# Optimization experiments

Hardware: AMD Instinct MI355X
Metric: run time of the kernel (lower is better)

Reference implementation:

```python
import jax, jax.numpy as jnp
import numpy as np

B, D, C = 128, 2048, 16522
BETA, KNN, ALPHA0 = 0.05, 6, 0.01


def setup_inputs() -> dict:
    key = jax.random.key(0)
    k1, k2, k3 = jax.random.split(key, 3)
    inputs = jax.random.normal(k1, (B, D), dtype=jnp.float32)
    label = jax.random.randint(k2, (B,), 0, C, dtype=jnp.int64 if jax.config.jax_enable_x64 else jnp.int32)
    # memory bank; init as unit-norm rows (torch init is zeros, but rows are
    # always renormalized after the first update, so unit-norm is the steady state)
    em = jax.random.normal(k3, (C, D), dtype=jnp.float32)
    em = em / jnp.linalg.norm(em, axis=1, keepdims=True)
    return {"inputs": inputs, "label": label, "em": em, "epoch": 10}


def reference(inputs, label, em, epoch):
    alpha = ALPHA0 * epoch
    # similarity logits: [B, C]
    logits = jnp.matmul(inputs, em.T) / BETA
    # smooth_hot mask: 2 at top-k entries, 3 at the true label (overwrites)
    _, topk = jax.lax.top_k(logits, KNN)                      # [B, KNN]
    rows = jnp.arange(B)
    mask = jnp.zeros_like(logits).at[rows[:, None], topk].set(2.0)
    mask = mask.at[rows, label].set(3.0)
    logp = jax.nn.log_softmax(logits, axis=1)
    loss = (-(mask * logp)).sum(axis=1).mean()
    # sequential per-sample EMA memory update (duplicate labels chain, so scan)
    def step(em_cur, xy):
        x, y = xy
        row = alpha * em_cur[y] + (1.0 - alpha) * x
        row = row / jnp.linalg.norm(row)
        return em_cur.at[y].set(row), None
    em_new, _ = jax.lax.scan(step, em, (inputs, label))
    return loss, em_new
```

## Files before the change

kernel.cpp:

```cpp
#include <hip/hip_runtime.h>
#include <hip/hip_bf16.h>
#include <cstddef>

#define B_    128
#define D_    2048
#define C_    16522
#define BETA_INV 20.0f
#define LSTRIDE 16528

#define NTILES 1033
#define NCHUNK 8
#define CHW    2066

typedef __bf16 bf16;
typedef bf16  bf16x8 __attribute__((ext_vector_type(8)));
typedef float f32x4  __attribute__((ext_vector_type(4)));

#define WS_APACK_OFF 8462336
#define WS_PART_OFF  8986624

__global__ __launch_bounds__(256) void pack_a(const float* __restrict__ inp,
                                              bf16* __restrict__ ap) {
  const int tid  = blockIdx.x * 256 + threadIdx.x;
  const int lane = tid & 63;
  const int ks   = (tid >> 6) & 63;
  const int mt   = tid >> 12;
  const int row  = mt * 16 + (lane & 15);
  const int col  = ks * 32 + (lane >> 4) * 8;
  const float4 v0 = *(const float4*)(inp + row * D_ + col);
  const float4 v1 = *(const float4*)(inp + row * D_ + col + 4);
  bf16x8 b;
  b[0] = (bf16)v0.x; b[1] = (bf16)v0.y; b[2] = (bf16)v0.z; b[3] = (bf16)v0.w;
  b[4] = (bf16)v1.x; b[5] = (bf16)v1.y; b[6] = (bf16)v1.z; b[7] = (bf16)v1.w;
  ((bf16x8*)ap)[tid] = b;
}

__global__ __launch_bounds__(256) void copy_em(const float* __restrict__ em,
                                               float* __restrict__ out_em) {
  const size_t n = (size_t)C_ * D_ / 4;
  const size_t stride = (size_t)gridDim.x * 512;
  for (size_t i = (size_t)blockIdx.x * 512 + threadIdx.x; i < n; i += stride) {
    const f32x4 v0 = ((const f32x4*)em)[i];
    const bool  h1 = (i + 256) < n;
    f32x4 v1 = {};
    if (h1) v1 = ((const f32x4*)em)[i + 256];
    ((f32x4*)out_em)[i] = v0;
    if (h1) ((f32x4*)out_em)[i + 256] = v1;
  }
}

__global__ __launch_bounds__(256, 4) void gemm_logits(
    const bf16*  __restrict__ ap,
    const float* __restrict__ em,
    float*       __restrict__ logits)
{
  const int tid  = threadIdx.x;
  const int lane = tid & 63;
  const int w    = tid >> 6;
  const int ml   = lane & 15;
  const int quad = lane >> 4;
  const int n0   = blockIdx.x * 16;
  const int r    = n0 + ml;
  const bool valid = r < C_;

  const float* bp = em + (size_t)(valid ? r : 0) * D_ + quad * 8;
  const bf16x8* af = (const bf16x8*)ap;

  const int ks0 = w * 16;

  f32x4 acc[8] = {};

  f32x4 e0a = *(const f32x4*)(bp + ks0 * 32);
  f32x4 e0b = *(const f32x4*)(bp + ks0 * 32 + 4);

  #pragma unroll 3
  for (int i = 0; i < 15; ++i) {
    const int ks = ks0 + i;
    bf16x8 A0[8];
    #pragma unroll
    for (int mt = 0; mt < 8; ++mt)
      A0[mt] = af[(mt * 64 + ks) * 64 + lane];
    const f32x4 e1a = *(const f32x4*)(bp + (ks + 1) * 32);
    const f32x4 e1b = *(const f32x4*)(bp + (ks + 1) * 32 + 4);
    bf16x8 bv;
    bv[0] = (bf16)e0a[0]; bv[1] = (bf16)e0a[1]; bv[2] = (bf16)e0a[2]; bv[3] = (bf16)e0a[3];
    bv[4] = (bf16)e0b[0]; bv[5] = (bf16)e0b[1]; bv[6] = (bf16)e0b[2]; bv[7] = (bf16)e0b[3];
    #pragma unroll
    for (int mt = 0; mt < 8; ++mt)
      acc[mt] = __builtin_amdgcn_mfma_f32_16x16x32_bf16(A0[mt], bv, acc[mt], 0, 0, 0);
    e0a = e1a; e0b = e1b;
  }
  {
    const int ks = ks0 + 15;
    bf16x8 A0[8];
    #pragma unroll
    for (int mt = 0; mt < 8; ++mt)
      A0[mt] = af[(mt * 64 + ks) * 64 + lane];
    bf16x8 bv;
    bv[0] = (bf16)e0a[0]; bv[1] = (bf16)e0a[1]; bv[2] = (bf16)e0a[2]; bv[3] = (bf16)e0a[3];
    bv[4] = (bf16)e0b[0]; bv[5] = (bf16)e0b[1]; bv[6] = (bf16)e0b[2]; bv[7] = (bf16)e0b[3];
    #pragma unroll
    for (int mt = 0; mt < 8; ++mt)
      acc[mt] = __builtin_amdgcn_mfma_f32_16x16x32_bf16(A0[mt], bv, acc[mt], 0, 0, 0);
  }

  __shared__ f32x4 red[3][8][64];
  if (w > 0) {
    #pragma unroll
    for (int mt = 0; mt < 8; ++mt) red[w - 1][mt][lane] = acc[mt];
  }
  __syncthreads();
  if (w == 0 && valid) {
    #pragma unroll
    for (int mt = 0; mt < 8; ++mt) {
      f32x4 a = acc[mt];
      a += red[0][mt][lane];
      a += red[1][mt][lane];
      a += red[2][mt][lane];
      #pragma unroll
      for (int reg = 0; reg < 4; ++reg) {
        const int row = mt * 16 + quad * 4 + reg;
        logits[row * LSTRIDE + r] = a[reg] * BETA_INV;
      }
    }
  }
}

__global__ __launch_bounds__(256) void row_loss_part(
    const float* __restrict__ logits,
    const int*   __restrict__ label,
    float*       __restrict__ part)
{
  const int b = blockIdx.x >> 3;
  const int c = blockIdx.x & 7;
  const int t = threadIdx.x;
  const int lo = c * CHW;
  const int hi = (lo + CHW < C_) ? lo + CHW : C_;
  const float* row = logits + b * LSTRIDE;
  const int y = label[b];

  float m = -INFINITY, s = 0.f, ly = -INFINITY;
  float tv[6]; int ti[6];
  #pragma unroll
  for (int q = 0; q < 6; ++q) { tv[q] = -INFINITY; ti[q] = -1; }

  for (int i = lo + t; i < hi; i += 256) {
    const float v = row[i];
    if (v > m) { s = s * __expf(m - v) + 1.f; m = v; }
    else       { s += __expf(v - m); }
    if (i == y) ly = v;
    if (v > tv[5]) {
      tv[5] = v; ti[5] = i;
      #pragma unroll
      for (int q = 5; q > 0; --q)
        if (tv[q] > tv[q - 1]) {
          const float fv = tv[q]; tv[q] = tv[q - 1]; tv[q - 1] = fv;
          const int   fi = ti[q]; ti[q] = ti[q - 1]; ti[q - 1] = fi;
        }
    }
  }

  __shared__ float rm[256], rs[256];
  __shared__ float cv[1536];
  __shared__ int   ci[1536];
  __shared__ float sly;

  rm[t] = m; rs[t] = s;
  #pragma unroll
  for (int q = 0; q < 6; ++q) { cv[t * 6 + q] = tv[q]; ci[t * 6 + q] = ti[q]; }
  if (t == 0) sly = -INFINITY;
  __syncthreads();
  if (ly != -INFINITY) sly = ly;

  for (int off = 128; off >= 1; off >>= 1) {
    if (t < off) {
      const float m2 = rm[t + off], s2 = rs[t + off];
      const float M = fmaxf(rm[t], m2);
      rs[t] = rs[t] * __expf(rm[t] - M) + s2 * __expf(m2 - M);
      rm[t] = M;
    }
    __syncthreads();
  }

  if (t < 64) {
    float otv[6]; int oti[6];
    for (int rr = 0; rr < 6; ++rr) {
      float bv = -INFINITY; int bi = -1, bs = -1;
      for (int u = 0; u < 24; ++u) {
        const int slot = t * 24 + u;
        const float v = cv[slot];
        if (v > bv) { bv = v; bi = ci[slot]; bs = slot; }
      }
      #pragma unroll
      for (int off = 32; off >= 1; off >>= 1) {
        const float ov = __shfl_down(bv, off);
        const int   oi = __shfl_down(bi, off);
        const int   os = __shfl_down(bs, off);
        if (ov > bv) { bv = ov; bi = oi; bs = os; }
      }
      bv = __shfl(bv, 0); bi = __shfl(bi, 0); bs = __shfl(bs, 0);
      if (bs >= t * 24 && bs < (t + 1) * 24) cv[bs] = -INFINITY;
      otv[rr] = bv; oti[rr] = bi;
    }
    if (t == 0) {
      float* p = part + (size_t)(b * 8 + c) * 16;
      p[0] = rm[0]; p[1] = rs[0]; p[2] = sly;
      #pragma unroll
      for (int q = 0; q < 6; ++q) { p[4 + q] = otv[q]; ((int*)p)[10 + q] = oti[q]; }
    }
  }
}

__global__ __launch_bounds__(64) void row_loss_merge(
    const float* __restrict__ part,
    const int*   __restrict__ label,
    float*       __restrict__ out)
{
  const int b = blockIdx.x;
  const int lane = threadIdx.x;
  const int y = label[b];

  float m = -INFINITY, s = 0.f, ly = -INFINITY;
  if (lane < 8) {
    const float* p = part + (size_t)(b * 8 + lane) * 16;
    m = p[0]; s = p[1]; ly = p[2];
  }
  float M = m, LY = ly;
  #pragma unroll
  for (int off = 32; off >= 1; off >>= 1) {
    M  = fmaxf(M,  __shfl_down(M,  off));
    LY = fmaxf(LY, __shfl_down(LY, off));
  }
  M = __shfl(M, 0); LY = __shfl(LY, 0);
  float contrib = (lane < 8) ? s * __expf(m - M) : 0.f;
  #pragma unroll
  for (int off = 32; off >= 1; off >>= 1) contrib += __shfl_down(contrib, off);
  const float S = __shfl(contrib, 0);

  float v = -INFINITY; int idx = -1;
  if (lane < 48) {
    const float* p = part + (size_t)(b * 8 + lane / 6) * 16;
    v   = p[4 + lane % 6];
    idx = ((const int*)p)[10 + lane % 6];
  }
  float stop = 0.f; int intop = 0;
  for (int rr = 0; rr < 6; ++rr) {
    float bv = v; int bi = idx, bl = lane;
    #pragma unroll
    for (int off = 32; off >= 1; off >>= 1) {
      const float ov = __shfl_down(bv, off);
      const int   oi = __shfl_down(bi, off);
      const int   ol = __shfl_down(bl, off);
      if (ov > bv) { bv = ov; bi = oi; bl = ol; }
    }
    bv = __shfl(bv, 0); bi = __shfl(bi, 0); bl = __shfl(bl, 0);
    stop += bv;
    if (bi == y) intop = 1;
    if (lane == bl) v = -INFINITY;
  }

  if (lane == 0) {
    const float lse = M + logf(S);
    const float loss = intop ? (13.f * lse - LY - 2.f * stop)
                             : (15.f * lse - 3.f * LY - 2.f * stop);
    atomicAdd(out, loss * (1.0f / 128.0f));
  }
}

__global__ __launch_bounds__(256) void em_update(
    const float* __restrict__ inp,
    const int*   __restrict__ label,
    const float* __restrict__ em,
    const int*   __restrict__ epoch,
    float*       __restrict__ out_em)
{
  __shared__ int lbl[B_];
  __shared__ float red[4];
  const int t = threadIdx.x;
  if (t < B_) lbl[t] = label[t];
  __syncthreads();

  const int i = blockIdx.x;
  const int y = lbl[i];
  for (int j = 0; j < i; ++j)
    if (lbl[j] == y) return;

  const float alpha = 0.01f * (float)epoch[0];
  const int lane = t & 63, wave = t >> 6;

  float r[8];
  #pragma unroll
  for (int u = 0; u < 8; ++u) r[u] = em[(size_t)y * D_ + t + u * 256];

  for (int j = i; j < B_; ++j) {
    if (lbl[j] != y) continue;
    const float* x = inp + j * D_;
    float ss = 0.f;
    #pragma unroll
    for (int u = 0; u < 8; ++u) {
      r[u] = alpha * r[u] + (1.f - alpha) * x[t + u * 256];
      ss += r[u] * r[u];
    }
    #pragma unroll
    for (int off = 32; off >= 1; off >>= 1) ss += __shfl_down(ss, off);
    if (lane == 0) red[wave] = ss;
    __syncthreads();
    const float inv = 1.f / sqrtf(red[0] + red[1] + red[2] + red[3]);
    #pragma unroll
    for (int u = 0; u < 8; ++u) r[u] *= inv;
    __syncthreads();
  }

  #pragma unroll
  for (int u = 0; u < 8; ++u) out_em[(size_t)y * D_ + t + u * 256] = r[u];
}

extern "C" void kernel_launch(void* const* d_in, const int* in_sizes, int n_in,
                              void* d_out, int out_size, void* d_ws, size_t ws_size,
                              hipStream_t stream) {
  const float* inp   = (const float*)d_in[0];
  const int*   label = (const int*)d_in[1];
  const float* em    = (const float*)d_in[2];
  const int*   epoch = (const int*)d_in[3];

  float* out    = (float*)d_out;
  float* out_em = out + 1;
  float* logits = (float*)d_ws;
  bf16*  apack  = (bf16*)((char*)d_ws + WS_APACK_OFF);
  float* part   = (float*)((char*)d_ws + WS_PART_OFF);

  hipMemsetAsync(d_out, 0, sizeof(float), stream);

  pack_a        <<<dim3(128),        dim3(256), 0, stream>>>(inp, apack);
  copy_em       <<<dim3(2048),       dim3(256), 0, stream>>>(em, out_em);
  gemm_logits   <<<dim3(NTILES),     dim3(256), 0, stream>>>(apack, em, logits);
  row_loss_part <<<dim3(B_ * NCHUNK),dim3(256), 0, stream>>>(logits, label, part);
  row_loss_merge<<<dim3(B_),         dim3(64),  0, stream>>>(part, label, out);
  em_update     <<<dim3(B_),         dim3(256), 0, stream>>>(inp, label, em, epoch, out_em);
}
```

Baseline: 130.3 us.

## Fuse em copy into GEMM launch and merge loss-merge with em update

Interleaves the memory-bank copy blocks with the GEMM tile blocks in one launch: of every three blocks, two copy and one computes a tile. The copy and the GEMM both stream em, so running them together can overlap the bandwidth-bound copy with compute and shares em reads in cache. The row-loss merge and the EMA update are also merged into one launch, which removes two kernel launches. The cost is a bigger, mixed kernel whose register budget is set by the GEMM path, and less control over block scheduling.

```diff
diff --git a/kernel.cpp b/kernel.cpp
--- a/kernel.cpp
+++ b/kernel.cpp
@@ -11,6 +11,9 @@
 #define NTILES 1033
 #define NCHUNK 8
 #define CHW    2066
+
+#define NCOPY  2066
+#define NFUSED 3099
 
 typedef __bf16 bf16;
 typedef bf16  bf16x8 __attribute__((ext_vector_type(8)));
@@ -35,31 +38,38 @@
   ((bf16x8*)ap)[tid] = b;
 }
 
-__global__ __launch_bounds__(256) void copy_em(const float* __restrict__ em,
-                                               float* __restrict__ out_em) {
-  const size_t n = (size_t)C_ * D_ / 4;
-  const size_t stride = (size_t)gridDim.x * 512;
-  for (size_t i = (size_t)blockIdx.x * 512 + threadIdx.x; i < n; i += stride) {
-    const f32x4 v0 = ((const f32x4*)em)[i];
-    const bool  h1 = (i + 256) < n;
-    f32x4 v1 = {};
-    if (h1) v1 = ((const f32x4*)em)[i + 256];
-    ((f32x4*)out_em)[i] = v0;
-    if (h1) ((f32x4*)out_em)[i + 256] = v1;
-  }
-}
-
-__global__ __launch_bounds__(256, 4) void gemm_logits(
+__global__ __launch_bounds__(256, 4) void fused_main(
+    const float* __restrict__ em,
+    float*       __restrict__ out_em,
     const bf16*  __restrict__ ap,
-    const float* __restrict__ em,
     float*       __restrict__ logits)
 {
+  const int b  = blockIdx.x;
+  const int g  = b / 3;
+  const int r3 = b - g * 3;
+
+  if (r3 < 2) {
+    const int id = g * 2 + r3;
+    const int t  = threadIdx.x;
+    const size_t n = (size_t)C_ * D_ / 4;
+    const size_t stride = (size_t)NCOPY * 512;
+    for (size_t i = (size_t)id * 512 + t; i < n; i += stride) {
+      const f32x4 v0 = ((const f32x4*)em)[i];
+      const bool  h1 = (i + 256) < n;
+      f32x4 v1 = {};
+      if (h1) v1 = ((const f32x4*)em)[i + 256];
+      ((f32x4*)out_em)[i] = v0;
+      if (h1) ((f32x4*)out_em)[i + 256] = v1;
+    }
+    return;
+  }
+
   const int tid  = threadIdx.x;
   const int lane = tid & 63;
   const int w    = tid >> 6;
   const int ml   = lane & 15;
   const int quad = lane >> 4;
-  const int n0   = blockIdx.x * 16;
+  const int n0   = g * 16;
   const int r    = n0 + ml;
   const bool valid = r < C_;
 
@@ -211,76 +221,77 @@
   }
 }
 
-__global__ __launch_bounds__(64) void row_loss_merge(
+__global__ __launch_bounds__(256) void tail(
     const float* __restrict__ part,
     const int*   __restrict__ label,
-    float*       __restrict__ out)
-{
-  const int b = blockIdx.x;
-  const int lane = threadIdx.x;
-  const int y = label[b];
-
-  float m = -INFINITY, s = 0.f, ly = -INFINITY;
-  if (lane < 8) {
-    const float* p = part + (size_t)(b * 8 + lane) * 16;
-    m = p[0]; s = p[1]; ly = p[2];
-  }
-  float M = m, LY = ly;
-  #pragma unroll
-  for (int off = 32; off >= 1; off >>= 1) {
-    M  = fmaxf(M,  __shfl_down(M,  off));
-    LY = fmaxf(LY, __shfl_down(LY, off));
-  }
-  M = __shfl(M, 0); LY = __shfl(LY, 0);
-  float contrib = (lane < 8) ? s * __expf(m - M) : 0.f;
-  #pragma unroll
-  for (int off = 32; off >= 1; off >>= 1) contrib += __shfl_down(contrib, off);
-  const float S = __shfl(contrib, 0);
-
-  float v = -INFINITY; int idx = -1;
-  if (lane < 48) {
-    const float* p = part + (size_t)(b * 8 + lane / 6) * 16;
-    v   = p[4 + lane % 6];
-    idx = ((const int*)p)[10 + lane % 6];
-  }
-  float stop = 0.f; int intop = 0;
-  for (int rr = 0; rr < 6; ++rr) {
-    float bv = v; int bi = idx, bl = lane;
-    #pragma unroll
-    for (int off = 32; off >= 1; off >>= 1) {
-      const float ov = __shfl_down(bv, off);
-      const int   oi = __shfl_down(bi, off);
-      const int   ol = __shfl_down(bl, off);
-      if (ov > bv) { bv = ov; bi = oi; bl = ol; }
-    }
-    bv = __shfl(bv, 0); bi = __shfl(bi, 0); bl = __shfl(bl, 0);
-    stop += bv;
-    if (bi == y) intop = 1;
-    if (lane == bl) v = -INFINITY;
-  }
-
-  if (lane == 0) {
-    const float lse = M + logf(S);
-    const float loss = intop ? (13.f * lse - LY - 2.f * stop)
-                             : (15.f * lse - 3.f * LY - 2.f * stop);
-    atomicAdd(out, loss * (1.0f / 128.0f));
-  }
-}
-
-__global__ __launch_bounds__(256) void em_update(
+    float*       __restrict__ out,
     const float* __restrict__ inp,
-    const int*   __restrict__ label,
     const float* __restrict__ em,
     const int*   __restrict__ epoch,
     float*       __restrict__ out_em)
 {
-  __shared__ int lbl[B_];
+  __shared__ int   lbl[B_];
   __shared__ float red[4];
+
+  if (blockIdx.x < 128) {
+    const int b = blockIdx.x;
+    const int lane = threadIdx.x;
+    if (lane >= 64) return;
+    const int y = label[b];
+
+    float m = -INFINITY, s = 0.f, ly = -INFINITY;
+    if (lane < 8) {
+      const float* p = part + (size_t)(b * 8 + lane) * 16;
+      m = p[0]; s = p[1]; ly = p[2];
+    }
+    float M = m, LY = ly;
+    #pragma unroll
+    for (int off = 32; off >= 1; off >>= 1) {
+      M  = fmaxf(M,  __shfl_down(M,  off));
+      LY = fmaxf(LY, __shfl_down(LY, off));
+    }
+    M = __shfl(M, 0); LY = __shfl(LY, 0);
+    float contrib = (lane < 8) ? s * __expf(m - M) : 0.f;
+    #pragma unroll
+    for (int off = 32; off >= 1; off >>= 1) contrib += __shfl_down(contrib, off);
+    const float S = __shfl(contrib, 0);
+
+    float v = -INFINITY; int idx = -1;
+    if (lane < 48) {
+      const float* p = part + (size_t)(b * 8 + lane / 6) * 16;
+      v   = p[4 + lane % 6];
+      idx = ((const int*)p)[10 + lane % 6];
+    }
+    float stop = 0.f; int intop = 0;
+    for (int rr = 0; rr < 6; ++rr) {
+      float bv = v; int bi = idx, bl = lane;
+      #pragma unroll
+      for (int off = 32; off >= 1; off >>= 1) {
+        const float ov = __shfl_down(bv, off);
+        const int   oi = __shfl_down(bi, off);
+        const int   ol = __shfl_down(bl, off);
+        if (ov > bv) { bv = ov; bi = oi; bl = ol; }
+      }
+      bv = __shfl(bv, 0); bi = __shfl(bi, 0); bl = __shfl(bl, 0);
+      stop += bv;
+      if (bi == y) intop = 1;
+      if (lane == bl) v = -INFINITY;
+    }
+
+    if (lane == 0) {
+      const float lse = M + logf(S);
+      const float loss = intop ? (13.f * lse - LY - 2.f * stop)
+                               : (15.f * lse - 3.f * LY - 2.f * stop);
+      atomicAdd(out, loss * (1.0f / 128.0f));
+    }
+    return;
+  }
+
   const int t = threadIdx.x;
   if (t < B_) lbl[t] = label[t];
   __syncthreads();
 
-  const int i = blockIdx.x;
+  const int i = blockIdx.x - 128;
   const int y = lbl[i];
   for (int j = 0; j < i; ++j)
     if (lbl[j] == y) return;
@@ -332,9 +343,7 @@
   hipMemsetAsync(d_out, 0, sizeof(float), stream);
 
   pack_a        <<<dim3(128),        dim3(256), 0, stream>>>(inp, apack);
-  copy_em       <<<dim3(2048),       dim3(256), 0, stream>>>(em, out_em);
-  gemm_logits   <<<dim3(NTILES),     dim3(256), 0, stream>>>(apack, em, logits);
+  fused_main    <<<dim3(NFUSED),     dim3(256), 0, stream>>>(em, out_em, apack, logits);
   row_loss_part <<<dim3(B_ * NCHUNK),dim3(256), 0, stream>>>(logits, label, part);
-  row_loss_merge<<<dim3(B_),         dim3(64),  0, stream>>>(part, label, out);
-  em_update     <<<dim3(B_),         dim3(256), 0, stream>>>(inp, label, em, epoch, out_em);
-}
+  tail          <<<dim3(256),        dim3(256), 0, stream>>>(part, label, out, inp, em, epoch, out_em);
+}
```

New measurement: 119.1 us. 8.6% less time.
